# Optimization experiments

Hardware: AMD Instinct MI355X
Metric: run time of the kernel (lower is better)

Reference implementation:

```python
import jax, jax.numpy as jnp
import numpy as np

TEMPERATURE = 0.1
LOSS_SCALE = 1.0
LAMBD = 0.5


def setup_inputs() -> dict:
    key = jax.random.key(0)
    k1, k2 = jax.random.split(key)
    B, D = 4096, 768
    predicted = jax.random.normal(k1, (B, D), dtype=jnp.float32)
    target = jax.random.normal(k2, (B, D), dtype=jnp.float32)
    return {"predicted": predicted, "target": target}


def reference(predicted, target):
    predicted = predicted.astype(jnp.float32)
    target = target.astype(jnp.float32)
    B = predicted.shape[0]

    # Pairwise L2 distances via Gram identity (avoids B x B x D intermediate):
    # ||p_i - t_j||^2 = ||p_i||^2 + ||t_j||^2 - 2 p_i . t_j
    p_sq = jnp.sum(predicted * predicted, axis=-1)  # [B]
    t_sq = jnp.sum(target * target, axis=-1)        # [B]
    cross = predicted @ target.T                    # [B, B]
    sq_dist = p_sq[:, None] + t_sq[None, :] - 2.0 * cross
    distances = jnp.sqrt(jnp.maximum(sq_dist, 0.0))  # [B, B]

    logits = -distances / TEMPERATURE
    # cross-entropy with labels = arange(B): mean of -log_softmax diagonal
    log_probs = jax.nn.log_softmax(logits, axis=-1)
    contrastive_dist_loss = -jnp.mean(jnp.diagonal(log_probs))

    # normalized L1 magnitude loss
    elementwise_l1 = jnp.sum(jnp.abs(predicted - target), axis=-1)  # [B]
    target_magnitude = jnp.sum(jnp.abs(target), axis=-1)            # [B]
    norm_factor = jax.lax.stop_gradient(target_magnitude)
    normalized_magnitude_loss = jnp.mean(elementwise_l1 / norm_factor)

    total_loss = LOSS_SCALE * (
        LAMBD * contrastive_dist_loss + (1.0 - LAMBD) * normalized_magnitude_loss
    )
    return (total_loss, contrastive_dist_loss, normalized_magnitude_loss)
```

## Files before the change

### kernel.cpp

```cpp
#include <hip/hip_runtime.h>
#include <hip/hip_bf16.h>
#include <math.h>

#define B_ROWS 4096
#define D_DIM  768

#define BM 128
#define BN 128
#define BK 32
#define NKT (D_DIM / BK)
#define KT_STRIDE (B_ROWS * 32)
#define NBLK ((B_ROWS / BM) * (B_ROWS / BN))

typedef __attribute__((ext_vector_type(8))) short bf16x8;
typedef __attribute__((ext_vector_type(4))) float f32x4;

__device__ __forceinline__ unsigned short f32_to_bf16(float x) {
    unsigned int u = __float_as_uint(x);
    return (unsigned short)((u + 0x7fffu + ((u >> 16) & 1u)) >> 16);
}

__global__ void __launch_bounds__(256) rowstats_kernel(
    const float* __restrict__ P, const float* __restrict__ T,
    unsigned short* __restrict__ Pb, unsigned short* __restrict__ Tb,
    float* __restrict__ p_sq, float* __restrict__ t_sq,
    float* __restrict__ diagl, float* __restrict__ magr,
    float* __restrict__ rowsum)
{
    const int wave = threadIdx.x >> 6, lane = threadIdx.x & 63;
    const int i = blockIdx.x * 4 + wave;
    const f32x4* prow = (const f32x4*)(P + (size_t)i * D_DIM);
    const f32x4* trow = (const f32x4*)(T + (size_t)i * D_DIM);
    const int swz = (i >> 1) & 3;

    float psq = 0.f, tsq = 0.f, cr = 0.f, l1 = 0.f, tm = 0.f;
    #pragma unroll
    for (int u = 0; u < 3; ++u) {
        const int c4 = u * 64 + lane;
        f32x4 p = prow[c4], t = trow[c4];
        #pragma unroll
        for (int k = 0; k < 4; ++k) {
            psq += p[k] * p[k]; tsq += t[k] * t[k]; cr += p[k] * t[k];
            l1 += fabsf(p[k] - t[k]); tm += fabsf(t[k]);
        }
        const int kt  = c4 >> 3;
        const int cc  = (c4 >> 1) & 3;
        const int sub = c4 & 1;
        const size_t doff = (size_t)kt * KT_STRIDE + (size_t)i * 32
                          + (size_t)(((cc ^ swz) << 3) + (sub << 2));
        *(ushort4*)(Pb + doff) = make_ushort4(f32_to_bf16(p[0]), f32_to_bf16(p[1]),
                                              f32_to_bf16(p[2]), f32_to_bf16(p[3]));
        *(ushort4*)(Tb + doff) = make_ushort4(f32_to_bf16(t[0]), f32_to_bf16(t[1]),
                                              f32_to_bf16(t[2]), f32_to_bf16(t[3]));
    }
    #pragma unroll
    for (int m = 1; m < 64; m <<= 1) {
        psq += __shfl_xor(psq, m, 64);
        tsq += __shfl_xor(tsq, m, 64);
        cr  += __shfl_xor(cr,  m, 64);
        l1  += __shfl_xor(l1,  m, 64);
        tm  += __shfl_xor(tm,  m, 64);
    }
    if (lane == 0) {
        p_sq[i] = psq;
        t_sq[i] = tsq;
        float sq = fmaxf(psq + tsq - 2.0f * cr, 0.0f);
        diagl[i] = -sqrtf(sq) * 10.0f;
        magr[i]  = l1 / tm;
        rowsum[i] = 0.0f;
    }
}

__global__ void __launch_bounds__(256, 3) lse_gemm_kernel(
    const unsigned short* __restrict__ Pb, const unsigned short* __restrict__ Tb,
    const float* __restrict__ p_sq, const float* __restrict__ t_sq,
    const float* __restrict__ diagl, float* __restrict__ rowsum)
{
    const int tid  = threadIdx.x;
    const int lane = tid & 63, wave = tid >> 6;

    const int flat = blockIdx.x;
    const int xcd  = flat & 7;
    const int s    = flat >> 3;
    const int ti   = ((xcd & 1) << 4) + (s & 15);
    const int tj   = ((xcd >> 1) << 3) + (s >> 4);
    const int i0   = ti * BM, j0 = tj * BN;

    const int wm = wave >> 1, wn = wave & 1;
    const int row16 = lane & 15, quad = lane >> 4;
    const int slot  = quad ^ ((row16 >> 1) & 3);

    const unsigned short* ap[4];
    const unsigned short* bp[4];
    #pragma unroll
    for (int mt = 0; mt < 4; ++mt)
        ap[mt] = Pb + (size_t)(i0 + wm * 64 + mt * 16 + row16) * 32 + slot * 8;
    #pragma unroll
    for (int nt = 0; nt < 4; ++nt)
        bp[nt] = Tb + (size_t)(j0 + wn * 64 + nt * 16 + row16) * 32 + slot * 8;

    f32x4 acc[4][4];
    #pragma unroll
    for (int a = 0; a < 4; ++a)
        #pragma unroll
        for (int b = 0; b < 4; ++b)
            acc[a][b] = (f32x4){0.f, 0.f, 0.f, 0.f};

    bf16x8 a0[4], b0[4], a1[4], b1[4];

    #pragma unroll
    for (int f = 0; f < 4; ++f) {
        a0[f] = *(const bf16x8*)(ap[f]);
        b0[f] = *(const bf16x8*)(bp[f]);
    }

    #pragma unroll
    for (int t = 0; t < NKT; t += 2) {
        {
            const size_t o1 = (size_t)(t + 1) * KT_STRIDE;
            #pragma unroll
            for (int f = 0; f < 4; ++f) {
                a1[f] = *(const bf16x8*)(ap[f] + o1);
                b1[f] = *(const bf16x8*)(bp[f] + o1);
            }
        }
        __builtin_amdgcn_s_setprio(1);
        #pragma unroll
        for (int mt = 0; mt < 4; ++mt)
            #pragma unroll
            for (int nt = 0; nt < 4; ++nt)
                acc[mt][nt] = __builtin_amdgcn_mfma_f32_16x16x32_bf16(
                    a0[mt], b0[nt], acc[mt][nt], 0, 0, 0);
        __builtin_amdgcn_s_setprio(0);

        if (t + 2 < NKT) {
            const size_t o2 = (size_t)(t + 2) * KT_STRIDE;
            #pragma unroll
            for (int f = 0; f < 4; ++f) {
                a0[f] = *(const bf16x8*)(ap[f] + o2);
                b0[f] = *(const bf16x8*)(bp[f] + o2);
            }
        }
        __builtin_amdgcn_s_setprio(1);
        #pragma unroll
        for (int mt = 0; mt < 4; ++mt)
            #pragma unroll
            for (int nt = 0; nt < 4; ++nt)
                acc[mt][nt] = __builtin_amdgcn_mfma_f32_16x16x32_bf16(
                    a1[mt], b1[nt], acc[mt][nt], 0, 0, 0);
        __builtin_amdgcn_s_setprio(0);
    }

    const float NT_LOG2E = -14.4269504089f;
    const float LOG2E    = 1.44269504089f;
    float tsq_l[4];
    #pragma unroll
    for (int nt = 0; nt < 4; ++nt)
        tsq_l[nt] = t_sq[j0 + wn * 64 + nt * 16 + row16];

    #pragma unroll
    for (int mt = 0; mt < 4; ++mt) {
        #pragma unroll
        for (int r = 0; r < 4; ++r) {
            const int i = i0 + wm * 64 + mt * 16 + quad * 4 + r;
            const float psq = p_sq[i];
            const float c0  = -diagl[i] * LOG2E;
            float sfin = 0.f;
            #pragma unroll
            for (int nt = 0; nt < 4; ++nt) {
                float c  = acc[mt][nt][r];
                float sq = fmaxf(fmaf(-2.0f, c, psq + tsq_l[nt]), 0.0f);
                float d  = sqrtf(sq);
                float y  = fmaf(d, NT_LOG2E, c0);
                sfin += exp2f(y);
            }
            #pragma unroll
            for (int m = 1; m < 16; m <<= 1) sfin += __shfl_xor(sfin, m, 64);
            if (row16 == 0) atomicAdd(&rowsum[i], sfin);
        }
    }
}

__global__ void __launch_bounds__(256) finalize_kernel(
    const float* __restrict__ rowsum, const float* __restrict__ magr,
    float* __restrict__ out)
{
    const int tid = threadIdx.x;
    double sc = 0.0, sm = 0.0;
    for (int i = tid; i < B_ROWS; i += 256) {
        sc += log((double)rowsum[i]);
        sm += (double)magr[i];
    }
    #pragma unroll
    for (int m = 1; m < 64; m <<= 1) {
        sc += __shfl_xor(sc, m, 64);
        sm += __shfl_xor(sm, m, 64);
    }
    __shared__ double red[4][2];
    const int wave = tid >> 6, lane = tid & 63;
    if (lane == 0) { red[wave][0] = sc; red[wave][1] = sm; }
    __syncthreads();
    if (tid == 0) {
        sc = red[0][0] + red[1][0] + red[2][0] + red[3][0];
        sm = red[0][1] + red[1][1] + red[2][1] + red[3][1];
        double lc = sc / (double)B_ROWS;
        double lm = sm / (double)B_ROWS;
        out[0] = (float)(0.5 * lc + 0.5 * lm);
        out[1] = (float)lc;
        out[2] = (float)lm;
    }
}

extern "C" void kernel_launch(void* const* d_in, const int* in_sizes, int n_in,
                              void* d_out, int out_size, void* d_ws, size_t ws_size,
                              hipStream_t stream) {
    const float* P = (const float*)d_in[0];
    const float* T = (const float*)d_in[1];
    float* out = (float*)d_out;

    char* ws = (char*)d_ws;
    float* rowsum = (float*)ws;               ws += B_ROWS * sizeof(float);
    float* p_sq   = (float*)ws;               ws += B_ROWS * sizeof(float);
    float* t_sq   = (float*)ws;               ws += B_ROWS * sizeof(float);
    float* diagl  = (float*)ws;               ws += B_ROWS * sizeof(float);
    float* magr   = (float*)ws;               ws += B_ROWS * sizeof(float);
    unsigned short* Pb = (unsigned short*)ws; ws += (size_t)B_ROWS * D_DIM * 2;
    unsigned short* Tb = (unsigned short*)ws;

    rowstats_kernel<<<B_ROWS / 4, 256, 0, stream>>>(
        P, T, Pb, Tb, p_sq, t_sq, diagl, magr, rowsum);
    lse_gemm_kernel<<<NBLK, 256, 0, stream>>>(
        Pb, Tb, p_sq, t_sq, diagl, rowsum);
    finalize_kernel<<<1, 256, 0, stream>>>(rowsum, magr, out);
}
```

Before: 121.2 us.

## Deepen GEMM register prefetch to three stages and retile block-to-XCD mapping

The LSE GEMM kernel moves from double-buffered to triple-buffered global-to-register prefetch, keeping loads two K-steps ahead of the MFMAs to hide more memory latency. The K loop is no longer fully unrolled. Occupancy drops from 3 to 2 workgroups per SIMD to make room for the extra registers. Each XCD's 128 tiles are now walked in two 8x8 passes instead of a 16x8 column sweep, to improve L2 reuse of the P and T tiles.

```diff
diff --git a/kernel.cpp b/kernel.cpp
--- a/kernel.cpp
+++ b/kernel.cpp
@@ -71,7 +71,7 @@
     }
 }
 
-__global__ void __launch_bounds__(256, 3) lse_gemm_kernel(
+__global__ void __launch_bounds__(256, 2) lse_gemm_kernel(
     const unsigned short* __restrict__ Pb, const unsigned short* __restrict__ Tb,
     const float* __restrict__ p_sq, const float* __restrict__ t_sq,
     const float* __restrict__ diagl, float* __restrict__ rowsum)
@@ -82,8 +82,10 @@
     const int flat = blockIdx.x;
     const int xcd  = flat & 7;
     const int s    = flat >> 3;
-    const int ti   = ((xcd & 1) << 4) + (s & 15);
-    const int tj   = ((xcd >> 1) << 3) + (s >> 4);
+    const int pass = s >> 6;
+    const int w    = s & 63;
+    const int ti   = ((xcd & 1) << 4) + (pass << 3) + (w >> 3);
+    const int tj   = ((xcd >> 1) << 3) + (w & 7);
     const int i0   = ti * BM, j0 = tj * BN;
 
     const int wm = wave >> 1, wn = wave & 1;
@@ -106,50 +108,41 @@
         for (int b = 0; b < 4; ++b)
             acc[a][b] = (f32x4){0.f, 0.f, 0.f, 0.f};
 
-    bf16x8 a0[4], b0[4], a1[4], b1[4];
-
-    #pragma unroll
-    for (int f = 0; f < 4; ++f) {
-        a0[f] = *(const bf16x8*)(ap[f]);
-        b0[f] = *(const bf16x8*)(bp[f]);
-    }
-
-    #pragma unroll
-    for (int t = 0; t < NKT; t += 2) {
-        {
-            const size_t o1 = (size_t)(t + 1) * KT_STRIDE;
-            #pragma unroll
-            for (int f = 0; f < 4; ++f) {
-                a1[f] = *(const bf16x8*)(ap[f] + o1);
-                b1[f] = *(const bf16x8*)(bp[f] + o1);
-            }
-        }
-        __builtin_amdgcn_s_setprio(1);
-        #pragma unroll
-        for (int mt = 0; mt < 4; ++mt)
-            #pragma unroll
-            for (int nt = 0; nt < 4; ++nt)
-                acc[mt][nt] = __builtin_amdgcn_mfma_f32_16x16x32_bf16(
-                    a0[mt], b0[nt], acc[mt][nt], 0, 0, 0);
-        __builtin_amdgcn_s_setprio(0);
-
-        if (t + 2 < NKT) {
-            const size_t o2 = (size_t)(t + 2) * KT_STRIDE;
-            #pragma unroll
-            for (int f = 0; f < 4; ++f) {
-                a0[f] = *(const bf16x8*)(ap[f] + o2);
-                b0[f] = *(const bf16x8*)(bp[f] + o2);
-            }
-        }
-        __builtin_amdgcn_s_setprio(1);
-        #pragma unroll
-        for (int mt = 0; mt < 4; ++mt)
-            #pragma unroll
-            for (int nt = 0; nt < 4; ++nt)
-                acc[mt][nt] = __builtin_amdgcn_mfma_f32_16x16x32_bf16(
-                    a1[mt], b1[nt], acc[mt][nt], 0, 0, 0);
-        __builtin_amdgcn_s_setprio(0);
-    }
+    bf16x8 a0[4], b0[4], a1[4], b1[4], a2[4], b2[4];
+
+#define LOADSET(A, B, T_)                                            \
+    {                                                                \
+        const size_t o_ = (size_t)(T_) * KT_STRIDE;                  \
+        _Pragma("unroll")                                            \
+        for (int f = 0; f < 4; ++f) {                                \
+            A[f] = *(const bf16x8*)(ap[f] + o_);                     \
+            B[f] = *(const bf16x8*)(bp[f] + o_);                     \
+        }                                                            \
+    }
+#define MFMASET(A, B)                                                \
+    __builtin_amdgcn_s_setprio(1);                                   \
+    _Pragma("unroll")                                                \
+    for (int mt = 0; mt < 4; ++mt)                                   \
+        _Pragma("unroll")                                            \
+        for (int nt = 0; nt < 4; ++nt)                               \
+            acc[mt][nt] = __builtin_amdgcn_mfma_f32_16x16x32_bf16(   \
+                A[mt], B[nt], acc[mt][nt], 0, 0, 0);                 \
+    __builtin_amdgcn_s_setprio(0);
+
+    LOADSET(a0, b0, 0)
+    LOADSET(a1, b1, 1)
+    LOADSET(a2, b2, 2)
+
+    for (int t = 0; t < NKT; t += 3) {
+        MFMASET(a0, b0)
+        if (t + 3 < NKT) LOADSET(a0, b0, t + 3)
+        MFMASET(a1, b1)
+        if (t + 4 < NKT) LOADSET(a1, b1, t + 4)
+        MFMASET(a2, b2)
+        if (t + 5 < NKT) LOADSET(a2, b2, t + 5)
+    }
+#undef LOADSET
+#undef MFMASET
 
     const float NT_LOG2E = -14.4269504089f;
     const float LOG2E    = 1.44269504089f;
```

Measured after the change: 127.9 us. 1.06x slower.
